# Kernel optimization log

Hardware: AMD Instinct MI355X
Metric: run time of the kernel (lower is better)

## Reference

```python
import jax, jax.numpy as jnp
import numpy as np

GAMMA = 1.0
DICE_EPS = 1.0


def setup_inputs() -> dict:
    key = jax.random.key(0)
    k1, k2, k3 = jax.random.split(key, 3)
    B, N, C = 32, 16384, 50
    predictions = jax.random.normal(k1, (B, N, C), dtype=jnp.float32)
    targets = jax.random.randint(k2, (B, N), 0, C, dtype=jnp.int64)
    pred_choice = jax.random.randint(k3, (B, N), 0, C, dtype=jnp.int64)
    return {"predictions": predictions, "targets": targets, "pred_choice": pred_choice}


def reference(predictions, targets, pred_choice):
    # predictions: [B, N, C] logits; targets, pred_choice: [B, N] int labels
    logp = jax.nn.log_softmax(predictions, axis=-1)              # [B, N, C]
    logp_t = jnp.take_along_axis(logp, targets[..., None], axis=-1)[..., 0]  # [B, N]
    ce_loss = -jnp.mean(logp_t)                                   # scalar (CrossEntropyLoss mean)

    # focal modulation: pn = softmax prob of the true class; loss = mean((1-pn)^gamma) * ce
    pn = jnp.exp(logp_t)                                          # [B, N]
    loss = jnp.mean((1.0 - pn) ** GAMMA) * ce_loss

    # dice: the per-class loop in the original reduces exactly to
    # top = total correct predictions, bot = 2 * total points
    tf = targets.reshape(-1)
    pf = pred_choice.reshape(-1)
    top = jnp.sum((pf == tf).astype(jnp.float32))
    bot = jnp.float32(2 * tf.shape[0])
    dice_loss = 1.0 - 2.0 * (top + DICE_EPS) / (bot + DICE_EPS)

    return loss + dice_loss
```

## Files before the change

### kernel.cpp

```cpp
#include <hip/hip_runtime.h>
#include <math.h>


#define NCLS 50
#define BLK 256

__global__ __launch_bounds__(BLK) void pnloss_main(
    const float* __restrict__ pred,
    const int* __restrict__ targets,
    const int* __restrict__ pchoice,
    float* __restrict__ partials,
    int rows, int nblocks)
{
    const int row = blockIdx.x * BLK + threadIdx.x;

    float logpt = 0.f, pn = 0.f, match = 0.f;

    if (row < rows) {
        const float2* rp = reinterpret_cast<const float2*>(pred + (size_t)row * NCLS);
        float2 v[NCLS / 2];
        #pragma unroll
        for (int j = 0; j < NCLS / 2; ++j) v[j] = rp[j];

        const int t = targets[row];

        float m = v[0].x;
        float xt = 0.f;
        #pragma unroll
        for (int j = 0; j < NCLS / 2; ++j) {
            m = fmaxf(m, fmaxf(v[j].x, v[j].y));
            xt = (t == 2 * j)     ? v[j].x : xt;
            xt = (t == 2 * j + 1) ? v[j].y : xt;
        }

        float s = 0.f;
        #pragma unroll
        for (int j = 0; j < NCLS / 2; ++j)
            s += __expf(v[j].x - m) + __expf(v[j].y - m);

        logpt = xt - m - __logf(s);
        pn    = __expf(logpt);
        match = (pchoice[row] == t) ? 1.f : 0.f;
    }

    #pragma unroll
    for (int off = 32; off > 0; off >>= 1) {
        logpt += __shfl_down(logpt, off);
        pn    += __shfl_down(pn, off);
        match += __shfl_down(match, off);
    }

    __shared__ float sm[3][BLK / 64];
    const int wid  = threadIdx.x >> 6;
    const int lane = threadIdx.x & 63;
    if (lane == 0) { sm[0][wid] = logpt; sm[1][wid] = pn; sm[2][wid] = match; }
    __syncthreads();

    if (threadIdx.x == 0) {
        float a = 0.f, b = 0.f, c = 0.f;
        #pragma unroll
        for (int w = 0; w < BLK / 64; ++w) { a += sm[0][w]; b += sm[1][w]; c += sm[2][w]; }
        partials[blockIdx.x]               = a;
        partials[blockIdx.x + nblocks]     = b;
        partials[blockIdx.x + 2 * nblocks] = c;
    }
}

__global__ __launch_bounds__(BLK) void pnloss_final(
    const float* __restrict__ partials,
    int nblocks, float inv_rows, float two_rows,
    float* __restrict__ out)
{
    float a = 0.f, b = 0.f, c = 0.f;
    for (int i = threadIdx.x; i < nblocks; i += BLK) {
        a += partials[i];
        b += partials[i + nblocks];
        c += partials[i + 2 * nblocks];
    }

    #pragma unroll
    for (int off = 32; off > 0; off >>= 1) {
        a += __shfl_down(a, off);
        b += __shfl_down(b, off);
        c += __shfl_down(c, off);
    }

    __shared__ float sm[3][BLK / 64];
    const int wid  = threadIdx.x >> 6;
    const int lane = threadIdx.x & 63;
    if (lane == 0) { sm[0][wid] = a; sm[1][wid] = b; sm[2][wid] = c; }
    __syncthreads();

    if (threadIdx.x == 0) {
        float sa = 0.f, sb = 0.f, sc = 0.f;
        #pragma unroll
        for (int w = 0; w < BLK / 64; ++w) { sa += sm[0][w]; sb += sm[1][w]; sc += sm[2][w]; }
        const float ce    = -sa * inv_rows;
        const float focal = 1.f - sb * inv_rows;
        const float loss  = focal * ce;
        const float dice  = 1.f - 2.f * (sc + 1.f) / (two_rows + 1.f);
        out[0] = loss + dice;
    }
}

extern "C" void kernel_launch(void* const* d_in, const int* in_sizes, int n_in,
                              void* d_out, int out_size, void* d_ws, size_t ws_size,
                              hipStream_t stream) {
    const float* pred    = (const float*)d_in[0];
    const int*   targets = (const int*)d_in[1];
    const int*   pchoice = (const int*)d_in[2];
    float*       out     = (float*)d_out;
    float*       partials = (float*)d_ws;

    const int rows    = in_sizes[1];
    const int nblocks = (rows + BLK - 1) / BLK;

    pnloss_main<<<nblocks, BLK, 0, stream>>>(pred, targets, pchoice, partials, rows, nblocks);
    pnloss_final<<<1, BLK, 0, stream>>>(partials, nblocks,
                                        1.0f / (float)rows, 2.0f * (float)rows, out);
}
```

Before: 27.08 us.

## Stage prediction tiles through LDS with coalesced float4 loads

Each block first cooperatively loads its 256 rows of logits into shared memory using coalesced float4 reads, then each thread processes its row from LDS. The target logit is indexed directly from LDS instead of a select chain. This targets the uncoalesced per-thread strided global reads, at the cost of a large LDS footprint that limits occupancy, possible bank conflicts on the 50-float row stride, and an extra barrier.

```diff
diff --git a/kernel.cpp b/kernel.cpp
--- a/kernel.cpp
+++ b/kernel.cpp
@@ -4,6 +4,9 @@
 
 #define NCLS 50
 #define BLK 256
+#define RPB 256
+#define NF4 (RPB * NCLS / 4)
+#define FULLK (NF4 / BLK)
 
 __global__ __launch_bounds__(BLK) void pnloss_main(
     const float* __restrict__ pred,
@@ -12,26 +15,49 @@
     float* __restrict__ partials,
     int rows, int nblocks)
 {
-    const int row = blockIdx.x * BLK + threadIdx.x;
+    __shared__ float sdata[RPB * NCLS];
 
+    const int tid = threadIdx.x;
+    const int rowbase = blockIdx.x * RPB;
+
+    if (rowbase + RPB <= rows) {
+        const float4* gp = reinterpret_cast<const float4*>(pred + (size_t)rowbase * NCLS);
+        float4* sp = reinterpret_cast<float4*>(sdata);
+
+        float4 tmp[FULLK];
+        #pragma unroll
+        for (int k = 0; k < FULLK; ++k) tmp[k] = gp[tid + k * BLK];
+        float4 tail;
+        const bool has_tail = tid < (NF4 - FULLK * BLK);
+        if (has_tail) tail = gp[tid + FULLK * BLK];
+
+        #pragma unroll
+        for (int k = 0; k < FULLK; ++k) sp[tid + k * BLK] = tmp[k];
+        if (has_tail) sp[tid + FULLK * BLK] = tail;
+    } else {
+        const size_t fbase = (size_t)rowbase * NCLS;
+        const size_t ftotal = (size_t)rows * NCLS;
+        for (int i = tid; i < RPB * NCLS; i += BLK) {
+            sdata[i] = (fbase + i < ftotal) ? pred[fbase + i] : 0.f;
+        }
+    }
+    __syncthreads();
+
+    const int row = rowbase + tid;
     float logpt = 0.f, pn = 0.f, match = 0.f;
 
     if (row < rows) {
-        const float2* rp = reinterpret_cast<const float2*>(pred + (size_t)row * NCLS);
+        const float2* rp = reinterpret_cast<const float2*>(sdata + tid * NCLS);
         float2 v[NCLS / 2];
         #pragma unroll
         for (int j = 0; j < NCLS / 2; ++j) v[j] = rp[j];
 
         const int t = targets[row];
+        const float xt = sdata[tid * NCLS + t];
 
         float m = v[0].x;
-        float xt = 0.f;
         #pragma unroll
-        for (int j = 0; j < NCLS / 2; ++j) {
-            m = fmaxf(m, fmaxf(v[j].x, v[j].y));
-            xt = (t == 2 * j)     ? v[j].x : xt;
-            xt = (t == 2 * j + 1) ? v[j].y : xt;
-        }
+        for (int j = 0; j < NCLS / 2; ++j) m = fmaxf(m, fmaxf(v[j].x, v[j].y));
 
         float s = 0.f;
         #pragma unroll
@@ -51,12 +77,12 @@
     }
 
     __shared__ float sm[3][BLK / 64];
-    const int wid  = threadIdx.x >> 6;
-    const int lane = threadIdx.x & 63;
+    const int wid  = tid >> 6;
+    const int lane = tid & 63;
     if (lane == 0) { sm[0][wid] = logpt; sm[1][wid] = pn; sm[2][wid] = match; }
     __syncthreads();
 
-    if (threadIdx.x == 0) {
+    if (tid == 0) {
         float a = 0.f, b = 0.f, c = 0.f;
         #pragma unroll
         for (int w = 0; w < BLK / 64; ++w) { a += sm[0][w]; b += sm[1][w]; c += sm[2][w]; }
@@ -106,14 +132,14 @@
 extern "C" void kernel_launch(void* const* d_in, const int* in_sizes, int n_in,
                               void* d_out, int out_size, void* d_ws, size_t ws_size,
                               hipStream_t stream) {
-    const float* pred    = (const float*)d_in[0];
-    const int*   targets = (const int*)d_in[1];
-    const int*   pchoice = (const int*)d_in[2];
-    float*       out     = (float*)d_out;
+    const float* pred     = (const float*)d_in[0];
+    const int*   targets  = (const int*)d_in[1];
+    const int*   pchoice  = (const int*)d_in[2];
+    float*       out      = (float*)d_out;
     float*       partials = (float*)d_ws;
 
     const int rows    = in_sizes[1];
-    const int nblocks = (rows + BLK - 1) / BLK;
+    const int nblocks = (rows + RPB - 1) / RPB;
 
     pnloss_main<<<nblocks, BLK, 0, stream>>>(pred, targets, pchoice, partials, rows, nblocks);
     pnloss_final<<<1, BLK, 0, stream>>>(partials, nblocks,
```

After: 26.39 us. -2.6%, faster.
